# Optimization experiments

Measured on AMD Instinct MI355X. Metric: run time of the kernel, lower is better.

## Reference

```python
import jax, jax.numpy as jnp
import numpy as np

N = 100000
E = 600000
DIM = 128
EDGE_DIM = 32

def setup_inputs() -> dict:
    key = jax.random.key(0)
    ks = jax.random.split(key, 10)
    s = 1.0 / np.sqrt(DIM)
    se = 1.0 / np.sqrt(EDGE_DIM)
    return {
        "x": jax.random.normal(ks[0], (N, DIM), dtype=jnp.float32),
        "edge_index": jax.random.randint(ks[1], (2, E), 0, N, dtype=jnp.int64),
        "edge_attr": jax.random.normal(ks[2], (E, EDGE_DIM), dtype=jnp.float32),
        "We": jax.random.uniform(ks[3], (EDGE_DIM, DIM), minval=-se, maxval=se, dtype=jnp.float32),
        "be": jnp.zeros((DIM,), dtype=jnp.float32),
        "W1": jax.random.uniform(ks[4], (DIM, DIM), minval=-s, maxval=s, dtype=jnp.float32),
        "b1": jnp.zeros((DIM,), dtype=jnp.float32),
        "W2": jax.random.uniform(ks[5], (DIM, DIM), minval=-s, maxval=s, dtype=jnp.float32),
        "b2": jnp.zeros((DIM,), dtype=jnp.float32),
        "eps": jnp.float32(0.0),
        "gamma": jnp.ones((DIM,), dtype=jnp.float32),
        "beta": jnp.zeros((DIM,), dtype=jnp.float32),
    }

def reference(x, edge_index, edge_attr, We, be, W1, b1, W2, b2, eps, gamma, beta):
    i, j = edge_index[0], edge_index[1]
    # gather source node features and add transformed edge features -> [E, dim]
    msg = x[j] + (edge_attr @ We + be)
    # scatter-sum aggregate to destination nodes -> [N, dim]
    agg = jax.ops.segment_sum(msg, i, num_segments=x.shape[0])
    h = (1.0 + eps) * x + agg
    # 2-layer MLP
    out = jax.nn.relu(h @ W1 + b1) @ W2 + b2
    # LayerNorm over last dim (dropout is identity in eval)
    mu = jnp.mean(out, axis=-1, keepdims=True)
    var = jnp.var(out, axis=-1, keepdims=True)
    out = (out - mu) * jax.lax.rsqrt(var + 1e-5) * gamma + beta
    return out
```

## Files before the change

kernel.cpp:

```cpp
#include <hip/hip_runtime.h>
#include <hip/hip_bf16.h>

#define N_NODES 100000
#define N_EDGES 600000
#define DIM 128
#define EDIM 32

typedef __attribute__((ext_vector_type(8))) short bf16x8;
typedef __attribute__((ext_vector_type(8))) short short8v;
typedef __attribute__((ext_vector_type(4))) float f32x4;

static __device__ __forceinline__ short f2bf(float v) {
    __hip_bfloat16 h = __float2bfloat16(v);
    return *(short*)&h;
}
static __device__ __forceinline__ float bfu2f(unsigned short u) {
    return __uint_as_float(((unsigned int)u) << 16);
}

#define HROW_OFF  0ULL
#define AGGE_OFF  25600000ULL
#define CSR_OFF   32000000ULL
#define OFF_OFF   36800000ULL
#define DEG_OFF   37200008ULL
#define BSUM_OFF  37600016ULL
#define WEW1_OFF  37600528ULL
#define XBF_OFF   37616912ULL
#define EBF_OFF   63216912ULL
#define SCAN_NBLK 98

__global__ __launch_bounds__(1024) void compute_wew1(
    const float* __restrict__ We, const float* __restrict__ W1,
    float* __restrict__ wew1) {
    const int idx = blockIdx.x * 1024 + threadIdx.x;
    const int k = idx >> 7, d2 = idx & 127;
    float a = 0.f;
    #pragma unroll 8
    for (int d = 0; d < DIM; ++d)
        a += We[k * DIM + d] * W1[d * DIM + d2];
    wew1[k * DIM + d2] = a;
}

__global__ __launch_bounds__(256) void cast_x_bf16(
    const float* __restrict__ x, unsigned short* __restrict__ xbf) {
    const int total = N_NODES * DIM / 8;
    for (int i = blockIdx.x * 256 + threadIdx.x; i < total; i += gridDim.x * 256) {
        float4 a = *(const float4*)&x[(size_t)i * 8];
        float4 b = *(const float4*)&x[(size_t)i * 8 + 4];
        short8v o;
        o[0] = f2bf(a.x); o[1] = f2bf(a.y); o[2] = f2bf(a.z); o[3] = f2bf(a.w);
        o[4] = f2bf(b.x); o[5] = f2bf(b.y); o[6] = f2bf(b.z); o[7] = f2bf(b.w);
        *(short8v*)&xbf[(size_t)i * 8] = o;
    }
}

__global__ __launch_bounds__(256) void cast_e_count(
    const float* __restrict__ eattr, unsigned short* __restrict__ ebf,
    const int* __restrict__ eidx, int* __restrict__ cnt) {
    const int total = N_EDGES * EDIM / 8;
    for (int i = blockIdx.x * 256 + threadIdx.x; i < total; i += gridDim.x * 256) {
        float4 a = *(const float4*)&eattr[(size_t)i * 8];
        float4 b = *(const float4*)&eattr[(size_t)i * 8 + 4];
        short8v o;
        o[0] = f2bf(a.x); o[1] = f2bf(a.y); o[2] = f2bf(a.z); o[3] = f2bf(a.w);
        o[4] = f2bf(b.x); o[5] = f2bf(b.y); o[6] = f2bf(b.z); o[7] = f2bf(b.w);
        *(short8v*)&ebf[(size_t)i * 8] = o;
        if (i < N_EDGES) atomicAdd(&cnt[eidx[i]], 1);
    }
}

__global__ __launch_bounds__(1024) void scan_blocks(
    const int* __restrict__ cnt, int* __restrict__ off, int* __restrict__ bsum) {
    const int t = blockIdx.x * 1024 + threadIdx.x;
    const int lane = threadIdx.x & 63, wv = threadIdx.x >> 6;
    int v = (t < N_NODES) ? cnt[t] : 0;
    int s = v;
    #pragma unroll
    for (int o = 1; o < 64; o <<= 1) {
        int u = __shfl_up(s, o, 64);
        if (lane >= o) s += u;
    }
    __shared__ int wsum[16];
    if (lane == 63) wsum[wv] = s;
    __syncthreads();
    if (threadIdx.x == 0) {
        int a = 0;
        #pragma unroll
        for (int w = 0; w < 16; ++w) { int tmp = wsum[w]; wsum[w] = a; a += tmp; }
        bsum[blockIdx.x] = a;
    }
    __syncthreads();
    if (t < N_NODES) off[t] = s - v + wsum[wv];
}

__global__ __launch_bounds__(1024) void scan_add2(
    int* __restrict__ off, int* __restrict__ cursor, const int* __restrict__ bsum) {
    __shared__ int pref;
    const int b = blockIdx.x;
    if (threadIdx.x < 64) {
        int v = 0;
        if ((int)threadIdx.x < b) v = bsum[threadIdx.x];
        const int i2 = threadIdx.x + 64;
        if (i2 < b) v += bsum[i2];
        #pragma unroll
        for (int o = 32; o >= 1; o >>= 1) v += __shfl_down(v, o, 64);
        if (threadIdx.x == 0) pref = v;
    }
    __syncthreads();
    const int t = b * 1024 + threadIdx.x;
    if (t < N_NODES) {
        const int val = off[t] + pref;
        off[t] = val;
        cursor[t] = val;
    } else if (t == N_NODES) {
        off[t] = N_EDGES;
    }
}

__global__ void csr_fill(const int* __restrict__ eidx, int* __restrict__ cursor,
                         int2* __restrict__ csr) {
    int e = blockIdx.x * 256 + threadIdx.x;
    if (e < N_EDGES) {
        int i = eidx[e];
        int p = atomicAdd(&cursor[i], 1);
        csr[p] = make_int2(e, eidx[N_EDGES + e]);
    }
}

__global__ __launch_bounds__(256, 8) void gine_aggregate(
    const unsigned short* __restrict__ xbf,
    const unsigned short* __restrict__ ebf,
    const int* __restrict__ off,
    const int2* __restrict__ csr,
    unsigned short* __restrict__ hrowG,
    unsigned short* __restrict__ aggE,
    const float* __restrict__ be,
    const float* __restrict__ epsp)
{
    const int l5 = threadIdx.x & 31;
    const int nhw = (gridDim.x * 256) >> 5;
    int n = (blockIdx.x * 256 + threadIdx.x) >> 5;
    const float epv = 1.0f + epsp[0];
    const float4 bev = ((const float4*)be)[l5];

    int s = off[n], e = off[n + 1];
    while (true) {
        const int n2 = n + nhw;
        int s2 = 0, e2 = 0;
        if (n2 < N_NODES) { s2 = off[n2]; e2 = off[n2 + 1]; }

        float a0 = 0.f, a1 = 0.f, a2 = 0.f, a3 = 0.f, ae = 0.f;
        for (int t0 = s; t0 < e; t0 += 8) {
            int2 cc[8];
            #pragma unroll
            for (int k = 0; k < 8; ++k)
                cc[k] = csr[min(t0 + k, e - 1)];
            ushort4 xv[8]; unsigned short ev[8];
            #pragma unroll
            for (int k = 0; k < 8; ++k) {
                xv[k] = *(const ushort4*)&xbf[(size_t)cc[k].y * DIM + l5 * 4];
                ev[k] = ebf[(size_t)cc[k].x * EDIM + l5];
            }
            #pragma unroll
            for (int k = 0; k < 8; ++k) {
                const float msk = (t0 + k < e) ? 1.f : 0.f;
                a0 += msk * bfu2f(xv[k].x); a1 += msk * bfu2f(xv[k].y);
                a2 += msk * bfu2f(xv[k].z); a3 += msk * bfu2f(xv[k].w);
                ae += msk * bfu2f(ev[k]);
            }
        }
        const float dgf = (float)(e - s);
        ushort4 xn = *(const ushort4*)&xbf[(size_t)n * DIM + l5 * 4];
        short4 hv;
        hv.x = f2bf(epv * bfu2f(xn.x) + a0 + dgf * bev.x);
        hv.y = f2bf(epv * bfu2f(xn.y) + a1 + dgf * bev.y);
        hv.z = f2bf(epv * bfu2f(xn.z) + a2 + dgf * bev.z);
        hv.w = f2bf(epv * bfu2f(xn.w) + a3 + dgf * bev.w);
        *(short4*)&hrowG[(size_t)n * DIM + l5 * 4] = hv;
        aggE[(size_t)n * EDIM + l5] = (unsigned short)f2bf(ae);

        if (n2 >= N_NODES) break;
        n = n2; s = s2; e = e2;
    }
}

#define HROW_STRIDE 136

__global__ __launch_bounds__(1024) void gine_mlp_fused(
    const unsigned short* __restrict__ hrowG,
    const unsigned short* __restrict__ aggE,
    const float* __restrict__ wew1,
    const float* __restrict__ W1,
    const float* __restrict__ b1,
    const float* __restrict__ W2,
    const float* __restrict__ b2,
    const float* __restrict__ gamma,
    const float* __restrict__ beta,
    float* __restrict__ out)
{
    __shared__ short Wp[2][16384];
    __shared__ short Wep[4096];
    __shared__ short hrow[16][16 * HROW_STRIDE];

    const int tid  = threadIdx.x;
    const int wave = tid >> 6;
    const int lane = tid & 63;
    const int m    = lane & 15;
    const int g    = lane >> 4;

    for (int s = wave * 2; s < wave * 2 + 2; ++s) {
        const int dt = s >> 2, kc = s & 3;
        const int krow = kc * 32 + g * 8;
        const int col  = dt * 16 + m;
        short p1[8], p2[8];
        #pragma unroll
        for (int j = 0; j < 8; ++j) {
            p1[j] = f2bf(W1[(size_t)(krow + j) * DIM + col]);
            p2[j] = f2bf(W2[(size_t)(krow + j) * DIM + col]);
        }
        #pragma unroll
        for (int j = 0; j < 8; ++j) {
            Wp[0][(s * 64 + lane) * 8 + j] = p1[j];
            Wp[1][(s * 64 + lane) * 8 + j] = p2[j];
        }
    }
    if (wave < 8) {
        const int dt = wave;
        const int col = dt * 16 + m;
        short pw[8];
        #pragma unroll
        for (int j = 0; j < 8; ++j) pw[j] = f2bf(wew1[(size_t)(g * 8 + j) * DIM + col]);
        #pragma unroll
        for (int j = 0; j < 8; ++j) Wep[(dt * 64 + lane) * 8 + j] = pw[j];
    }

    float b1v[8], b2v[8], gv[8], btv[8];
    #pragma unroll
    for (int dt = 0; dt < 8; ++dt) {
        const int d = dt * 16 + m;
        b1v[dt] = b1[d]; b2v[dt] = b2[d]; gv[dt] = gamma[d]; btv[dt] = beta[d];
    }
    __syncthreads();

    short* myrow = &hrow[wave][0];
    const int ntiles = N_NODES / 16;

    for (int tile = blockIdx.x * 16 + wave; tile < ntiles; tile += gridDim.x * 16) {
        const int nbase = tile * 16;

        bf16x8 afragE = *(const bf16x8*)&aggE[(size_t)(nbase + m) * EDIM + g * 8];

        #pragma unroll
        for (int r = 0; r < 4; ++r) {
            const int idx8 = r * 64 + lane;
            const int node = idx8 >> 4, dc = idx8 & 15;
            short8v v = *(const short8v*)&hrowG[(size_t)(nbase + node) * DIM + dc * 8];
            *(short8v*)&myrow[node * HROW_STRIDE + dc * 8] = v;
        }
        __asm__ volatile("s_waitcnt lgkmcnt(0)" ::: "memory");

        f32x4 acc[8];
        #pragma unroll
        for (int dt = 0; dt < 8; ++dt) {
            bf16x8 bfrag = *(bf16x8*)&Wep[(dt * 64 + lane) * 8];
            acc[dt] = __builtin_amdgcn_mfma_f32_16x16x32_bf16(
                afragE, bfrag, (f32x4){0.f, 0.f, 0.f, 0.f}, 0, 0, 0);
        }
        #pragma unroll
        for (int kc = 0; kc < 4; ++kc) {
            bf16x8 afrag = *(bf16x8*)&myrow[m * HROW_STRIDE + kc * 32 + g * 8];
            #pragma unroll
            for (int dt = 0; dt < 8; ++dt) {
                bf16x8 bfrag = *(bf16x8*)&Wp[0][((dt * 4 + kc) * 64 + lane) * 8];
                acc[dt] = __builtin_amdgcn_mfma_f32_16x16x32_bf16(afrag, bfrag, acc[dt], 0, 0, 0);
            }
        }
        __asm__ volatile("s_waitcnt lgkmcnt(0)" ::: "memory");

        #pragma unroll
        for (int dt = 0; dt < 8; ++dt)
            #pragma unroll
            for (int q = 0; q < 4; ++q) {
                float v = fmaxf(acc[dt][q] + b1v[dt], 0.f);
                myrow[(g * 4 + q) * HROW_STRIDE + dt * 16 + m] = f2bf(v);
            }
        __asm__ volatile("s_waitcnt lgkmcnt(0)" ::: "memory");

        #pragma unroll
        for (int dt = 0; dt < 8; ++dt) acc[dt] = (f32x4){0.f, 0.f, 0.f, 0.f};
        #pragma unroll
        for (int kc = 0; kc < 4; ++kc) {
            bf16x8 afrag = *(bf16x8*)&myrow[m * HROW_STRIDE + kc * 32 + g * 8];
            #pragma unroll
            for (int dt = 0; dt < 8; ++dt) {
                bf16x8 bfrag = *(bf16x8*)&Wp[1][((dt * 4 + kc) * 64 + lane) * 8];
                acc[dt] = __builtin_amdgcn_mfma_f32_16x16x32_bf16(afrag, bfrag, acc[dt], 0, 0, 0);
            }
        }

        float s[4] = {0, 0, 0, 0}, ss[4] = {0, 0, 0, 0};
        #pragma unroll
        for (int dt = 0; dt < 8; ++dt)
            #pragma unroll
            for (int q = 0; q < 4; ++q) {
                float o = acc[dt][q] + b2v[dt];
                acc[dt][q] = o;
                s[q] += o; ss[q] += o * o;
            }
        #pragma unroll
        for (int mask = 1; mask < 16; mask <<= 1)
            #pragma unroll
            for (int q = 0; q < 4; ++q) {
                s[q]  += __shfl_xor(s[q], mask, 64);
                ss[q] += __shfl_xor(ss[q], mask, 64);
            }
        float mu[4], inv[4];
        #pragma unroll
        for (int q = 0; q < 4; ++q) {
            mu[q] = s[q] * (1.0f / DIM);
            float var = ss[q] * (1.0f / DIM) - mu[q] * mu[q];
            inv[q] = rsqrtf(var + 1e-5f);
        }
        #pragma unroll
        for (int dt = 0; dt < 8; ++dt)
            #pragma unroll
            for (int q = 0; q < 4; ++q) {
                const int node = nbase + g * 4 + q;
                out[(size_t)node * DIM + dt * 16 + m] =
                    (acc[dt][q] - mu[q]) * inv[q] * gv[dt] + btv[dt];
            }
    }
}

extern "C" void kernel_launch(void* const* d_in, const int* in_sizes, int n_in,
                              void* d_out, int out_size, void* d_ws, size_t ws_size,
                              hipStream_t stream) {
    const float* x     = (const float*)d_in[0];
    const int*   eidx  = (const int*)d_in[1];
    const float* eattr = (const float*)d_in[2];
    const float* We    = (const float*)d_in[3];
    const float* be    = (const float*)d_in[4];
    const float* W1    = (const float*)d_in[5];
    const float* b1    = (const float*)d_in[6];
    const float* W2    = (const float*)d_in[7];
    const float* b2v   = (const float*)d_in[8];
    const float* eps   = (const float*)d_in[9];
    const float* gamma = (const float*)d_in[10];
    const float* beta  = (const float*)d_in[11];
    float* out = (float*)d_out;

    char* ws = (char*)d_ws;
    unsigned short* hrowG = (unsigned short*)(ws + HROW_OFF);
    unsigned short* aggE  = (unsigned short*)(ws + AGGE_OFF);
    int2*  csr  = (int2*)(ws + CSR_OFF);
    int*   off  = (int*)(ws + OFF_OFF);
    int*   cnt  = (int*)(ws + DEG_OFF);
    int*   bsum = (int*)(ws + BSUM_OFF);
    float* wew1 = (float*)(ws + WEW1_OFF);
    unsigned short* xbf = (unsigned short*)(ws + XBF_OFF);
    unsigned short* ebf = (unsigned short*)(ws + EBF_OFF);

    (void)hipMemsetAsync(cnt, 0, 400000, stream);
    compute_wew1<<<4, 1024, 0, stream>>>(We, W1, wew1);
    cast_x_bf16<<<2048, 256, 0, stream>>>(x, xbf);
    cast_e_count<<<2048, 256, 0, stream>>>(eattr, ebf, eidx, cnt);
    scan_blocks<<<SCAN_NBLK, 1024, 0, stream>>>(cnt, off, bsum);
    scan_add2<<<SCAN_NBLK, 1024, 0, stream>>>(off, cnt, bsum);
    csr_fill<<<(N_EDGES + 255) / 256, 256, 0, stream>>>(eidx, cnt, csr);
    gine_aggregate<<<2048, 256, 0, stream>>>(xbf, ebf, off, csr, hrowG, aggE, be, eps);
    gine_mlp_fused<<<256, 1024, 0, stream>>>(hrowG, aggE, wew1,
                                             W1, b1, W2, b2v, gamma, beta, out);
}
```

Measured before the change: 362.1 us.

## Fuse small setup kernels to cut launch count

Folds the count-buffer memset into the x cast kernel, replaces the two-kernel multi-block prefix scan with a single-block chunked scan, and computes the We·W1 product inside the MLP kernel's prologue instead of a separate kernel. The aim is to remove launch and dependency overhead of tiny kernels. In exchange, the scan runs serially on one block with strided uncoalesced accesses, and every MLP block redundantly recomputes the 32x128 product.

```diff
diff --git a/kernel.cpp b/kernel.cpp
--- a/kernel.cpp
+++ b/kernel.cpp
@@ -23,28 +23,16 @@
 #define CSR_OFF   32000000ULL
 #define OFF_OFF   36800000ULL
 #define DEG_OFF   37200008ULL
-#define BSUM_OFF  37600016ULL
-#define WEW1_OFF  37600528ULL
 #define XBF_OFF   37616912ULL
 #define EBF_OFF   63216912ULL
-#define SCAN_NBLK 98
-
-__global__ __launch_bounds__(1024) void compute_wew1(
-    const float* __restrict__ We, const float* __restrict__ W1,
-    float* __restrict__ wew1) {
-    const int idx = blockIdx.x * 1024 + threadIdx.x;
-    const int k = idx >> 7, d2 = idx & 127;
-    float a = 0.f;
-    #pragma unroll 8
-    for (int d = 0; d < DIM; ++d)
-        a += We[k * DIM + d] * W1[d * DIM + d2];
-    wew1[k * DIM + d2] = a;
-}
-
-__global__ __launch_bounds__(256) void cast_x_bf16(
-    const float* __restrict__ x, unsigned short* __restrict__ xbf) {
+
+__global__ __launch_bounds__(256) void cast_x_zero(
+    const float* __restrict__ x, unsigned short* __restrict__ xbf,
+    int* __restrict__ cnt) {
+    const int tid = blockIdx.x * 256 + threadIdx.x;
+    if (tid < N_NODES) cnt[tid] = 0;
     const int total = N_NODES * DIM / 8;
-    for (int i = blockIdx.x * 256 + threadIdx.x; i < total; i += gridDim.x * 256) {
+    for (int i = tid; i < total; i += gridDim.x * 256) {
         float4 a = *(const float4*)&x[(size_t)i * 8];
         float4 b = *(const float4*)&x[(size_t)i * 8 + 4];
         short8v o;
@@ -69,52 +57,43 @@
     }
 }
 
-__global__ __launch_bounds__(1024) void scan_blocks(
-    const int* __restrict__ cnt, int* __restrict__ off, int* __restrict__ bsum) {
-    const int t = blockIdx.x * 1024 + threadIdx.x;
-    const int lane = threadIdx.x & 63, wv = threadIdx.x >> 6;
-    int v = (t < N_NODES) ? cnt[t] : 0;
-    int s = v;
+__global__ __launch_bounds__(1024) void scan_fused(
+    const int* __restrict__ cnt, int* __restrict__ off, int* __restrict__ cursor) {
+    const int t = threadIdx.x;
+    const int CHUNK = (N_NODES + 1023) / 1024;
+    const int base = t * CHUNK;
+    int sum = 0;
+    for (int k = 0; k < CHUNK; ++k) {
+        const int idx = base + k;
+        if (idx < N_NODES) sum += cnt[idx];
+    }
+    const int lane = t & 63, wv = t >> 6;
+    int s = sum;
     #pragma unroll
     for (int o = 1; o < 64; o <<= 1) {
         int u = __shfl_up(s, o, 64);
         if (lane >= o) s += u;
     }
-    __shared__ int wsum[16];
+    __shared__ int wsum[16], wpre[16];
     if (lane == 63) wsum[wv] = s;
     __syncthreads();
-    if (threadIdx.x == 0) {
+    if (t == 0) {
         int a = 0;
         #pragma unroll
-        for (int w = 0; w < 16; ++w) { int tmp = wsum[w]; wsum[w] = a; a += tmp; }
-        bsum[blockIdx.x] = a;
+        for (int w = 0; w < 16; ++w) { wpre[w] = a; a += wsum[w]; }
     }
     __syncthreads();
-    if (t < N_NODES) off[t] = s - v + wsum[wv];
-}
-
-__global__ __launch_bounds__(1024) void scan_add2(
-    int* __restrict__ off, int* __restrict__ cursor, const int* __restrict__ bsum) {
-    __shared__ int pref;
-    const int b = blockIdx.x;
-    if (threadIdx.x < 64) {
-        int v = 0;
-        if ((int)threadIdx.x < b) v = bsum[threadIdx.x];
-        const int i2 = threadIdx.x + 64;
-        if (i2 < b) v += bsum[i2];
-        #pragma unroll
-        for (int o = 32; o >= 1; o >>= 1) v += __shfl_down(v, o, 64);
-        if (threadIdx.x == 0) pref = v;
-    }
-    __syncthreads();
-    const int t = b * 1024 + threadIdx.x;
-    if (t < N_NODES) {
-        const int val = off[t] + pref;
-        off[t] = val;
-        cursor[t] = val;
-    } else if (t == N_NODES) {
-        off[t] = N_EDGES;
-    }
+    int pre = s - sum + wpre[wv];
+    for (int k = 0; k < CHUNK; ++k) {
+        const int idx = base + k;
+        if (idx < N_NODES) {
+            const int c = cnt[idx];
+            off[idx] = pre;
+            cursor[idx] = pre;
+            pre += c;
+        }
+    }
+    if (t == 1023) off[N_NODES] = N_EDGES;
 }
 
 __global__ void csr_fill(const int* __restrict__ eidx, int* __restrict__ cursor,
@@ -189,7 +168,7 @@
 __global__ __launch_bounds__(1024) void gine_mlp_fused(
     const unsigned short* __restrict__ hrowG,
     const unsigned short* __restrict__ aggE,
-    const float* __restrict__ wew1,
+    const float* __restrict__ We,
     const float* __restrict__ W1,
     const float* __restrict__ b1,
     const float* __restrict__ W2,
@@ -224,14 +203,21 @@
             Wp[1][(s * 64 + lane) * 8 + j] = p2[j];
         }
     }
-    if (wave < 8) {
-        const int dt = wave;
-        const int col = dt * 16 + m;
-        short pw[8];
-        #pragma unroll
-        for (int j = 0; j < 8; ++j) pw[j] = f2bf(wew1[(size_t)(g * 8 + j) * DIM + col]);
-        #pragma unroll
-        for (int j = 0; j < 8; ++j) Wep[(dt * 64 + lane) * 8 + j] = pw[j];
+    {
+        const int k  = tid >> 5;
+        const int c0 = (tid & 31) * 4;
+        float a4[4] = {0.f, 0.f, 0.f, 0.f};
+        for (int d = 0; d < DIM; ++d) {
+            const float w = We[k * DIM + d];
+            const float4 r = *(const float4*)&W1[(size_t)d * DIM + c0];
+            a4[0] += w * r.x; a4[1] += w * r.y; a4[2] += w * r.z; a4[3] += w * r.w;
+        }
+        const int gk = k >> 3, jk = k & 7;
+        #pragma unroll
+        for (int q = 0; q < 4; ++q) {
+            const int col = c0 + q;
+            Wep[((((col >> 4) * 64) + gk * 16 + (col & 15)) << 3) + jk] = f2bf(a4[q]);
+        }
     }
 
     float b1v[8], b2v[8], gv[8], btv[8];
@@ -355,19 +341,14 @@
     int2*  csr  = (int2*)(ws + CSR_OFF);
     int*   off  = (int*)(ws + OFF_OFF);
     int*   cnt  = (int*)(ws + DEG_OFF);
-    int*   bsum = (int*)(ws + BSUM_OFF);
-    float* wew1 = (float*)(ws + WEW1_OFF);
     unsigned short* xbf = (unsigned short*)(ws + XBF_OFF);
     unsigned short* ebf = (unsigned short*)(ws + EBF_OFF);
 
-    (void)hipMemsetAsync(cnt, 0, 400000, stream);
-    compute_wew1<<<4, 1024, 0, stream>>>(We, W1, wew1);
-    cast_x_bf16<<<2048, 256, 0, stream>>>(x, xbf);
+    cast_x_zero<<<2048, 256, 0, stream>>>(x, xbf, cnt);
     cast_e_count<<<2048, 256, 0, stream>>>(eattr, ebf, eidx, cnt);
-    scan_blocks<<<SCAN_NBLK, 1024, 0, stream>>>(cnt, off, bsum);
-    scan_add2<<<SCAN_NBLK, 1024, 0, stream>>>(off, cnt, bsum);
+    scan_fused<<<1, 1024, 0, stream>>>(cnt, off, cnt);
     csr_fill<<<(N_EDGES + 255) / 256, 256, 0, stream>>>(eidx, cnt, csr);
     gine_aggregate<<<2048, 256, 0, stream>>>(xbf, ebf, off, csr, hrowG, aggE, be, eps);
-    gine_mlp_fused<<<256, 1024, 0, stream>>>(hrowG, aggE, wew1,
+    gine_mlp_fused<<<256, 1024, 0, stream>>>(hrowG, aggE, We,
                                              W1, b1, W2, b2v, gamma, beta, out);
 }
```

New measurement: 601.8 us. 66.2% more time.
